# Optimization experiments

Measured on AMD Instinct MI355X. Metric: run time of the kernel, lower is better.

## Reference

```python
import jax, jax.numpy as jnp
import numpy as np
import math

HASHMAP_SIZE = 1 << 17
N_LEVELS = 16
N_FEATURES = 2
BASE_RES = 16.0
GROWTH = 1.5  # per-level resolution growth factor
PRIME_Y = np.uint32(2654435761)  # Instant-NGP spatial hash prime


def hash_encode(x, encoding):
    """Multiresolution 2D hash-grid encoding with bilinear interpolation.
    x: [N, 2] in [0,1); encoding: [T, L, F]. Returns [N, L*F]."""
    N = x.shape[0]
    scales = jnp.asarray(BASE_RES * GROWTH ** np.arange(N_LEVELS),
                         dtype=x.dtype)  # [L]
    pos = x[:, None, :] * scales[None, :, None]        # [N, L, 2]
    pf = jnp.floor(pos)
    frac = pos - pf                                    # [N, L, 2]
    pi = pf.astype(jnp.uint32)                         # integer corner base
    lvl = jnp.arange(N_LEVELS)[None, :]                # [1, L]

    feat = jnp.zeros((N, N_LEVELS, N_FEATURES), dtype=x.dtype)
    for cx in (0, 1):
        for cy in (0, 1):
            ix = pi[..., 0] + jnp.uint32(cx)
            iy = pi[..., 1] + jnp.uint32(cy)
            h = ix ^ (iy * PRIME_Y)                    # spatial hash (wraps mod 2^32)
            idx = (h & jnp.uint32(HASHMAP_SIZE - 1)).astype(jnp.int32)  # [N, L]
            wx = frac[..., 0] if cx else 1.0 - frac[..., 0]
            wy = frac[..., 1] if cy else 1.0 - frac[..., 1]
            feat = feat + (wx * wy)[..., None] * encoding[idx, lvl]  # gather [N,L,F]
    return feat.reshape(N, N_LEVELS * N_FEATURES)


def setup_inputs() -> dict:
    key = jax.random.key(0)
    ks = jax.random.split(key, 8)
    N = 1 << 20
    n_neurons = [32, 64, 64, 3]
    x = jax.random.uniform(ks[0], (N, 2), dtype=jnp.float32)
    # encoding init: rand * 2e-4 - 1e-4
    encoding = jax.random.uniform(ks[1], (HASHMAP_SIZE, N_LEVELS, N_FEATURES),
                                  dtype=jnp.float32) * 2e-4 - 1e-4
    inp = {"x": x, "encoding": encoding}
    for i in range(3):
        s = 1.0 / math.sqrt(n_neurons[i])
        w = jax.random.uniform(ks[2 + i], (n_neurons[i], n_neurons[i + 1]),
                               dtype=jnp.float32) * 2 * s - s
        b = jax.random.uniform(ks[5 + i], (n_neurons[i + 1],),
                               dtype=jnp.float32) * 2 * s - s
        inp[f"w{i}"] = w
        inp[f"b{i}"] = b
    return inp


def reference(x, encoding, w0, b0, w1, b1, w2, b2):
    feat = hash_encode(x, encoding)                 # [N, 32]
    h = jax.nn.relu(feat @ w0 + b0)                 # [N, 64]
    h = jax.nn.relu(h @ w1 + b1)                    # [N, 64]
    return h @ w2 + b2                              # [N, 3]
```

## Files before the change

### kernel.cpp

```cpp
#include <hip/hip_runtime.h>
#include <stdint.h>

typedef __bf16 bf16_t;
typedef bf16_t bf16x8 __attribute__((ext_vector_type(8)));
typedef float  f32x4  __attribute__((ext_vector_type(4)));
typedef float  f32x2v __attribute__((ext_vector_type(2)));

static constexpr uint32_t PRIME = 2654435761u;
static constexpr uint32_t HMASK = (1u << 17) - 1u;
static constexpr uint32_t TSIZE = 1u << 17;

static constexpr int NLDS   = 5308;
static constexpr int NDALL  = 136642;

static constexpr float FSCALE = 8192.0f;
static constexpr float WSCALE = 1.0f / 8192.0f;

__device__ __forceinline__ uint32_t fbits(float f) {
    union { float f; uint32_t u; } v; v.f = f; return v.u;
}
__device__ __forceinline__ float asfloat(uint32_t u) {
    union { uint32_t u; float f; } v; v.u = u; return v.f;
}

__device__ __forceinline__ uint32_t enc8(float v) {
    const uint32_t s = (fbits(v) >> 24) & 0x80u;
    float m = fabsf(v) * 0x1p-120f;
    uint32_t u = fbits(m);
    u += 0x7FFFFu + ((u >> 20) & 1u);
    return s | ((u >> 20) & 0x7fu);
}
__device__ __forceinline__ uint32_t pack8(float a, float b) {
#if __has_builtin(__builtin_amdgcn_cvt_pk_fp8_f32)
    return (uint32_t)__builtin_amdgcn_cvt_pk_fp8_f32(a, b, 0, false) & 0xffffu;
#else
    return enc8(a) | (enc8(b) << 8);
#endif
}
template <bool HI>
__device__ __forceinline__ float2 unpack8w(uint32_t u) {
#if __has_builtin(__builtin_amdgcn_cvt_pk_f32_fp8)
    f32x2v r = __builtin_amdgcn_cvt_pk_f32_fp8((int)u, HI);
    return make_float2(r.x, r.y);
#else
    const uint32_t w = HI ? (u >> 16) : (u & 0xffffu);
    const float f0 = asfloat(((w & 0x80u) << 24) | ((w & 0x7fu) << 20)) * 0x1p120f;
    const float f1 = asfloat(((w & 0x8000u) << 16) | ((w & 0x7f00u) << 12)) * 0x1p120f;
    return make_float2(f0, f1);
#endif
}

__global__ __launch_bounds__(256)
void prepass_all(const float2* __restrict__ src, uint16_t* __restrict__ tab8,
                 uint16_t* __restrict__ dense) {
    __shared__ uint16_t ldsT[8 * 257];
    const int tid = threadIdx.x;
    if (blockIdx.x < 512) {
        const int t0 = blockIdx.x * 256;
#pragma unroll
        for (int k = 0; k < 8; ++k) {
            const int j = k * 256 + tid;
            const int tl = j >> 3, l8 = j & 7;
            const float2 f = src[((size_t)(t0 + tl) << 4) + 8 + l8];
            ldsT[l8 * 257 + tl] = (uint16_t)pack8(f.x * FSCALE, f.y * FSCALE);
        }
        __syncthreads();
#pragma unroll
        for (int k = 0; k < 8; ++k)
            tab8[((uint32_t)k << 17) + t0 + tid] = ldsT[k * 257 + tid];
    } else {
        const int i = (blockIdx.x - 512) * 256 + tid;
        if (i >= NDALL) return;
        int lvl, W, off;
        if      (i <   289) { lvl = 0; W =  17; off = 0;     }
        else if (i <   914) { lvl = 1; W =  25; off = 289;   }
        else if (i <  2283) { lvl = 2; W =  37; off = 914;   }
        else if (i <  5308) { lvl = 3; W =  55; off = 2283;  }
        else if (i < 12032) { lvl = 4; W =  82; off = 5308;  }
        else if (i < 27161) { lvl = 5; W = 123; off = 12032; }
        else if (i < 61017) { lvl = 6; W = 184; off = 27161; }
        else                { lvl = 7; W = 275; off = 61017; }
        const int li = i - off;
        const uint32_t iy = (uint32_t)(li / W), ix = (uint32_t)(li % W);
        const uint32_t h = (ix ^ (iy * PRIME)) & HMASK;
        const float2 f = src[h * 16 + lvl];
        dense[i] = (uint16_t)pack8(f.x * FSCALE, f.y * FSCALE);
    }
}

__global__ __launch_bounds__(256, 2)
void fused_hash_mlp(const float* __restrict__ xin,
                    const uint16_t* __restrict__ tab8,
                    const uint16_t* __restrict__ dense,
                    const float* __restrict__ w0, const float* __restrict__ b0,
                    const float* __restrict__ w1, const float* __restrict__ b1,
                    const float* __restrict__ w2, const float* __restrict__ b2,
                    float* __restrict__ out,
                    int nGroups)
{
    __shared__ uint16_t ldsTab[NLDS];
    __shared__ __align__(16) bf16_t lds[4 * 16 * 64];

    const int tid  = threadIdx.x;
    const int wib  = tid >> 6;
    const int lane = tid & 63;
    const int q    = lane >> 4;
    const int n16  = lane & 15;
    const int m7   = n16 & 7;
    const int mb   = n16 >> 3;

    bf16_t* myLds = &lds[wib * (16 * 64)];

    for (int i = tid; i < NLDS; i += 256) ldsTab[i] = dense[i];

    bf16x8 Bw0[4], Bw1[2][4], Bw2[2];
#pragma unroll
    for (int t = 0; t < 4; ++t)
#pragma unroll
        for (int j = 0; j < 8; ++j)
            Bw0[t][j] = (bf16_t)(w0[(q * 8 + j) * 64 + t * 16 + n16] * WSCALE);
#pragma unroll
    for (int c = 0; c < 2; ++c)
#pragma unroll
        for (int t = 0; t < 4; ++t)
#pragma unroll
            for (int j = 0; j < 8; ++j)
                Bw1[c][t][j] = (bf16_t)w1[(c * 32 + q * 8 + j) * 64 + t * 16 + n16];
#pragma unroll
    for (int c = 0; c < 2; ++c)
#pragma unroll
        for (int j = 0; j < 8; ++j)
            Bw2[c][j] = (n16 < 3) ? (bf16_t)w2[(c * 32 + q * 8 + j) * 3 + n16]
                                  : (bf16_t)0.0f;

    float bv0[4], bv1[4];
#pragma unroll
    for (int t = 0; t < 4; ++t) {
        bv0[t] = b0[t * 16 + n16];
        bv1[t] = b1[t * 16 + n16];
    }
    const float bv2 = (n16 < 3) ? b2[n16] : 0.0f;

    const float sb = 16.0f * ((q == 0) ? 1.0f :
                              (q == 1) ? 5.0625f :
                              (q == 2) ? 25.62890625f :
                                         129.746337890625f);
    const float sc[4] = { sb, sb * 1.5f, sb * 2.25f, sb * 3.375f };

    const uint32_t l8base = ((uint32_t)((q >= 2 ? q - 2 : 0) * 4)) << 17;

    int wbase[4];
#pragma unroll
    for (int r = 0; r < 4; ++r)
        wbase[r] = (q * 4 + r) * 64 + m7 + ((mb ^ (r & 1)) << 3) + ((q & 1) << 5);
    const int rIdx0 = n16 * 64 + (( q      ^ m7) << 3);
    const int rIdx1 = n16 * 64 + (((4 + q) ^ m7) << 3);

    __syncthreads();

    for (int g = blockIdx.x; g < nGroups; g += gridDim.x) {
        const int tile = g * 4 + wib;
        const int p = tile * 16 + n16;
        const float2 xy = ((const float2*)xin)[p];
        const float px = xy.x, py = xy.y;

        bf16x8 af;
#pragma unroll
        for (int lv = 0; lv < 4; ++lv) {
            const float posx = px * sc[lv], posy = py * sc[lv];
            const float fx = floorf(posx), fy = floorf(posy);
            const float frx = posx - fx,  fry = posy - fy;
            const uint32_t ix = (uint32_t)fx, iy = (uint32_t)fy;

            const uint32_t Wl = (lv == 0) ? 17u  : (lv == 1) ? 25u
                              : (lv == 2) ? 37u  : 55u;
            const uint32_t Ol = (lv == 0) ? 0u   : (lv == 1) ? 289u
                              : (lv == 2) ? 914u : 2283u;
            const uint32_t Wg = (lv == 0) ? 82u    : (lv == 1) ? 123u
                              : (lv == 2) ? 184u   : 275u;
            const uint32_t Og = (lv == 0) ? 5308u  : (lv == 1) ? 12032u
                              : (lv == 2) ? 27161u : 61017u;

            uint32_t u00, u10, u01, u11;
            if (q == 0) {
                const uint32_t a = Ol + iy * Wl + ix;
                u00 = ldsTab[a];
                u10 = ldsTab[a + 1];
                u01 = ldsTab[a + Wl];
                u11 = ldsTab[a + Wl + 1];
            } else if (q == 1) {
                const uint32_t a = Og + iy * Wg + ix;
                u00 = dense[a];
                u10 = dense[a + 1];
                u01 = dense[a + Wg];
                u11 = dense[a + Wg + 1];
            } else {
                const uint32_t hy0 = iy * PRIME, hy1 = hy0 + PRIME;
                const uint32_t i00 = ( ix       ^ hy0) & HMASK;
                const uint32_t i10 = ((ix + 1u) ^ hy0) & HMASK;
                const uint32_t i01 = ( ix       ^ hy1) & HMASK;
                const uint32_t i11 = ((ix + 1u) ^ hy1) & HMASK;
                const uint32_t base = l8base + ((uint32_t)lv << 17);
                u00 = tab8[base + i00];
                u10 = tab8[base + i10];
                u01 = tab8[base + i01];
                u11 = tab8[base + i11];
            }

            const float2 e00 = unpack8w<false>(u00);
            const float2 e10 = unpack8w<false>(u10);
            const float2 e01 = unpack8w<false>(u01);
            const float2 e11 = unpack8w<false>(u11);
            const float wx1 = frx, wx0 = 1.0f - frx, wy1 = fry, wy0 = 1.0f - fry;
            const float w00 = wx0 * wy0, w10 = wx1 * wy0, w01 = wx0 * wy1, w11 = wx1 * wy1;
            const float f0 = w00 * e00.x + w10 * e10.x + w01 * e01.x + w11 * e11.x;
            const float f1 = w00 * e00.y + w10 * e10.y + w01 * e01.y + w11 * e11.y;
            af[2 * lv]     = (bf16_t)f0;
            af[2 * lv + 1] = (bf16_t)f1;
        }

        f32x4 c0[4];
#pragma unroll
        for (int t = 0; t < 4; ++t) {
            f32x4 cc = { bv0[t], bv0[t], bv0[t], bv0[t] };
            c0[t] = __builtin_amdgcn_mfma_f32_16x16x32_bf16(af, Bw0[t], cc, 0, 0, 0);
        }

#pragma unroll
        for (int t = 0; t < 4; ++t)
#pragma unroll
            for (int r = 0; r < 4; ++r) {
                const int idx = ((t < 2) ? wbase[r] : (wbase[r] ^ 32))
                              + ((((t & 1) ^ ((r >> 1) & 1))) << 4);
                myLds[idx] = (bf16_t)fmaxf(c0[t][r], 0.0f);
            }
        bf16x8 A1[2];
        A1[0] = *(const bf16x8*)&myLds[rIdx0];
        A1[1] = *(const bf16x8*)&myLds[rIdx1];

        f32x4 c1[4];
#pragma unroll
        for (int t = 0; t < 4; ++t) {
            f32x4 cc = { bv1[t], bv1[t], bv1[t], bv1[t] };
            cc    = __builtin_amdgcn_mfma_f32_16x16x32_bf16(A1[0], Bw1[0][t], cc, 0, 0, 0);
            c1[t] = __builtin_amdgcn_mfma_f32_16x16x32_bf16(A1[1], Bw1[1][t], cc, 0, 0, 0);
        }

#pragma unroll
        for (int t = 0; t < 4; ++t)
#pragma unroll
            for (int r = 0; r < 4; ++r) {
                const int idx = ((t < 2) ? wbase[r] : (wbase[r] ^ 32))
                              + ((((t & 1) ^ ((r >> 1) & 1))) << 4);
                myLds[idx] = (bf16_t)fmaxf(c1[t][r], 0.0f);
            }
        bf16x8 A2[2];
        A2[0] = *(const bf16x8*)&myLds[rIdx0];
        A2[1] = *(const bf16x8*)&myLds[rIdx1];

        f32x4 co = { bv2, bv2, bv2, bv2 };
        co = __builtin_amdgcn_mfma_f32_16x16x32_bf16(A2[0], Bw2[0], co, 0, 0, 0);
        co = __builtin_amdgcn_mfma_f32_16x16x32_bf16(A2[1], Bw2[1], co, 0, 0, 0);

        if (n16 < 3) {
#pragma unroll
            for (int r = 0; r < 4; ++r)
                out[(size_t)(tile * 16 + q * 4 + r) * 3 + n16] = co[r];
        }
    }
}

__global__ __launch_bounds__(256)
void fused_hash_mlp_fp32(const float* __restrict__ xin,
                         const float* __restrict__ enc,
                         const float* __restrict__ w0, const float* __restrict__ b0,
                         const float* __restrict__ w1, const float* __restrict__ b1,
                         const float* __restrict__ w2, const float* __restrict__ b2,
                         float* __restrict__ out,
                         int nGroups)
{
    __shared__ __align__(16) bf16_t lds[4 * 16 * 80];
    const int tid  = threadIdx.x;
    const int wib  = tid >> 6;
    const int lane = tid & 63;
    const int q    = lane >> 4;
    const int n16  = lane & 15;
    bf16_t* myLds = &lds[wib * (16 * 80)];

    bf16x8 Bw0[4], Bw1[2][4], Bw2[2];
#pragma unroll
    for (int t = 0; t < 4; ++t)
#pragma unroll
        for (int j = 0; j < 8; ++j)
            Bw0[t][j] = (bf16_t)w0[(q * 8 + j) * 64 + t * 16 + n16];
#pragma unroll
    for (int c = 0; c < 2; ++c)
#pragma unroll
        for (int t = 0; t < 4; ++t)
#pragma unroll
            for (int j = 0; j < 8; ++j)
                Bw1[c][t][j] = (bf16_t)w1[(c * 32 + q * 8 + j) * 64 + t * 16 + n16];
#pragma unroll
    for (int c = 0; c < 2; ++c)
#pragma unroll
        for (int j = 0; j < 8; ++j)
            Bw2[c][j] = (n16 < 3) ? (bf16_t)w2[(c * 32 + q * 8 + j) * 3 + n16]
                                  : (bf16_t)0.0f;

    float bv0[4], bv1[4];
#pragma unroll
    for (int t = 0; t < 4; ++t) { bv0[t] = b0[t * 16 + n16]; bv1[t] = b1[t * 16 + n16]; }
    const float bv2 = (n16 < 3) ? b2[n16] : 0.0f;

    const float sb = 16.0f * ((q == 0) ? 1.0f : (q == 1) ? 5.0625f :
                              (q == 2) ? 25.62890625f : 129.746337890625f);
    const float sc[4] = { sb, sb * 1.5f, sb * 2.25f, sb * 3.375f };
    const char* encB = (const char*)enc;
    const uint32_t lvBase = (uint32_t)q * 32u;

    for (int g = blockIdx.x; g < nGroups; g += gridDim.x) {
        const int tile = g * 4 + wib;
        const int p = tile * 16 + n16;
        const float2 xy = ((const float2*)xin)[p];
        const float px = xy.x, py = xy.y;

        bf16x8 af;
#pragma unroll
        for (int lv = 0; lv < 4; ++lv) {
            const float posx = px * sc[lv], posy = py * sc[lv];
            const float fx = floorf(posx), fy = floorf(posy);
            const float frx = posx - fx,  fry = posy - fy;
            const uint32_t ix = (uint32_t)fx, iy = (uint32_t)fy;
            const uint32_t hy0 = iy * PRIME, hy1 = hy0 + PRIME;
            const uint32_t i00 = ( ix       ^ hy0) & HMASK;
            const uint32_t i10 = ((ix + 1u) ^ hy0) & HMASK;
            const uint32_t i01 = ( ix       ^ hy1) & HMASK;
            const uint32_t i11 = ((ix + 1u) ^ hy1) & HMASK;
            const uint32_t off = lvBase + (uint32_t)lv * 8u;
            const float2 e00 = *(const float2*)(encB + (i00 * 128u + off));
            const float2 e10 = *(const float2*)(encB + (i10 * 128u + off));
            const float2 e01 = *(const float2*)(encB + (i01 * 128u + off));
            const float2 e11 = *(const float2*)(encB + (i11 * 128u + off));
            const float wx1 = frx, wx0 = 1.0f - frx, wy1 = fry, wy0 = 1.0f - fry;
            const float w00 = wx0 * wy0, w10 = wx1 * wy0, w01 = wx0 * wy1, w11 = wx1 * wy1;
            af[2 * lv]     = (bf16_t)(w00 * e00.x + w10 * e10.x + w01 * e01.x + w11 * e11.x);
            af[2 * lv + 1] = (bf16_t)(w00 * e00.y + w10 * e10.y + w01 * e01.y + w11 * e11.y);
        }

        f32x4 c0[4];
#pragma unroll
        for (int t = 0; t < 4; ++t) {
            f32x4 cc = { bv0[t], bv0[t], bv0[t], bv0[t] };
            c0[t] = __builtin_amdgcn_mfma_f32_16x16x32_bf16(af, Bw0[t], cc, 0, 0, 0);
        }
        __syncthreads();
#pragma unroll
        for (int t = 0; t < 4; ++t)
#pragma unroll
            for (int r = 0; r < 4; ++r)
                myLds[(q * 4 + r) * 80 + t * 16 + n16] = (bf16_t)fmaxf(c0[t][r], 0.0f);
        __syncthreads();
        bf16x8 A1[2];
#pragma unroll
        for (int c = 0; c < 2; ++c)
            A1[c] = *(const bf16x8*)&myLds[n16 * 80 + c * 32 + q * 8];

        f32x4 c1[4];
#pragma unroll
        for (int t = 0; t < 4; ++t) {
            f32x4 cc = { bv1[t], bv1[t], bv1[t], bv1[t] };
            cc    = __builtin_amdgcn_mfma_f32_16x16x32_bf16(A1[0], Bw1[0][t], cc, 0, 0, 0);
            c1[t] = __builtin_amdgcn_mfma_f32_16x16x32_bf16(A1[1], Bw1[1][t], cc, 0, 0, 0);
        }
        __syncthreads();
#pragma unroll
        for (int t = 0; t < 4; ++t)
#pragma unroll
            for (int r = 0; r < 4; ++r)
                myLds[(q * 4 + r) * 80 + t * 16 + n16] = (bf16_t)fmaxf(c1[t][r], 0.0f);
        __syncthreads();
        bf16x8 A2[2];
#pragma unroll
        for (int c = 0; c < 2; ++c)
            A2[c] = *(const bf16x8*)&myLds[n16 * 80 + c * 32 + q * 8];

        f32x4 co = { bv2, bv2, bv2, bv2 };
        co = __builtin_amdgcn_mfma_f32_16x16x32_bf16(A2[0], Bw2[0], co, 0, 0, 0);
        co = __builtin_amdgcn_mfma_f32_16x16x32_bf16(A2[1], Bw2[1], co, 0, 0, 0);
        if (n16 < 3) {
#pragma unroll
            for (int r = 0; r < 4; ++r)
                out[(size_t)(tile * 16 + q * 4 + r) * 3 + n16] = co[r];
        }
    }
}

extern "C" void kernel_launch(void* const* d_in, const int* in_sizes, int n_in,
                              void* d_out, int out_size, void* d_ws, size_t ws_size,
                              hipStream_t stream) {
    const float* x  = (const float*)d_in[0];
    const float* en = (const float*)d_in[1];
    const float* w0 = (const float*)d_in[2];
    const float* b0 = (const float*)d_in[3];
    const float* w1 = (const float*)d_in[4];
    const float* b1 = (const float*)d_in[5];
    const float* w2 = (const float*)d_in[6];
    const float* b2 = (const float*)d_in[7];
    float* out = (float*)d_out;

    const int N = in_sizes[0] / 2;
    const int nTiles = N / 16;
    const int nGroups = nTiles / 4;

    const size_t wsNeeded = ((size_t)TSIZE * 8 + NDALL) * 2;
    if (ws_size >= wsNeeded) {
        uint16_t* tab8  = (uint16_t*)d_ws;
        uint16_t* dense = tab8 + ((size_t)TSIZE * 8);
        const int preBlocks = 512 + (NDALL + 255) / 256;
        prepass_all<<<preBlocks, 256, 0, stream>>>((const float2*)en, tab8, dense);
        int blocks = 2048;
        if (blocks > nGroups) blocks = nGroups;
        fused_hash_mlp<<<blocks, 256, 0, stream>>>(x, tab8, dense,
                                                   w0, b0, w1, b1, w2, b2, out, nGroups);
    } else {
        int blocks = 2048;
        if (blocks > nGroups) blocks = nGroups;
        fused_hash_mlp_fp32<<<blocks, 256, 0, stream>>>(x, en, w0, b0, w1, b1, w2, b2, out, nGroups);
    }
}
```

Measured before the change: 198.9 us.

## Stage MLP weights in LDS and raise occupancy target to cut VGPR pressure

Result: slower. 493.5 us (+148.1%).

```diff
diff --git a/kernel.cpp b/kernel.cpp
--- a/kernel.cpp
+++ b/kernel.cpp
@@ -10,7 +10,6 @@
 static constexpr uint32_t HMASK = (1u << 17) - 1u;
 static constexpr uint32_t TSIZE = 1u << 17;
 
-static constexpr int NLDS   = 5308;
 static constexpr int NDALL  = 136642;
 
 static constexpr float FSCALE = 8192.0f;
@@ -88,7 +87,7 @@
     }
 }
 
-__global__ __launch_bounds__(256, 2)
+__global__ __launch_bounds__(256, 8)
 void fused_hash_mlp(const float* __restrict__ xin,
                     const uint16_t* __restrict__ tab8,
                     const uint16_t* __restrict__ dense,
@@ -98,8 +97,8 @@
                     float* __restrict__ out,
                     int nGroups)
 {
-    __shared__ uint16_t ldsTab[NLDS];
     __shared__ __align__(16) bf16_t lds[4 * 16 * 64];
+    __shared__ __align__(16) bf16_t wLds[12 * 64 * 8];
 
     const int tid  = threadIdx.x;
     const int wib  = tid >> 6;
@@ -111,28 +110,33 @@
 
     bf16_t* myLds = &lds[wib * (16 * 64)];
 
-    for (int i = tid; i < NLDS; i += 256) ldsTab[i] = dense[i];
-
-    bf16x8 Bw0[4], Bw1[2][4], Bw2[2];
-#pragma unroll
-    for (int t = 0; t < 4; ++t)
-#pragma unroll
-        for (int j = 0; j < 8; ++j)
-            Bw0[t][j] = (bf16_t)(w0[(q * 8 + j) * 64 + t * 16 + n16] * WSCALE);
-#pragma unroll
-    for (int c = 0; c < 2; ++c)
-#pragma unroll
-        for (int t = 0; t < 4; ++t)
+    {
+        bf16x8 tmp;
+#pragma unroll
+        for (int t = 0; t < 4; ++t) {
 #pragma unroll
             for (int j = 0; j < 8; ++j)
-                Bw1[c][t][j] = (bf16_t)w1[(c * 32 + q * 8 + j) * 64 + t * 16 + n16];
+                tmp[j] = (bf16_t)(w0[(q * 8 + j) * 64 + t * 16 + n16] * WSCALE);
+            if (wib == 0) *(bf16x8*)&wLds[(t * 64 + lane) * 8] = tmp;
+        }
+#pragma unroll
+        for (int c = 0; c < 2; ++c)
+#pragma unroll
+            for (int t = 0; t < 4; ++t) {
+#pragma unroll
+                for (int j = 0; j < 8; ++j)
+                    tmp[j] = (bf16_t)w1[(c * 32 + q * 8 + j) * 64 + t * 16 + n16];
+                if (wib == 0) *(bf16x8*)&wLds[((4 + c * 4 + t) * 64 + lane) * 8] = tmp;
+            }
+    }
+
+    bf16x8 Bw2[2];
 #pragma unroll
     for (int c = 0; c < 2; ++c)
 #pragma unroll
         for (int j = 0; j < 8; ++j)
             Bw2[c][j] = (n16 < 3) ? (bf16_t)w2[(c * 32 + q * 8 + j) * 3 + n16]
                                   : (bf16_t)0.0f;
-
     float bv0[4], bv1[4];
 #pragma unroll
     for (int t = 0; t < 4; ++t) {
@@ -182,18 +186,14 @@
                               : (lv == 2) ? 27161u : 61017u;
 
             uint32_t u00, u10, u01, u11;
-            if (q == 0) {
-                const uint32_t a = Ol + iy * Wl + ix;
-                u00 = ldsTab[a];
-                u10 = ldsTab[a + 1];
-                u01 = ldsTab[a + Wl];
-                u11 = ldsTab[a + Wl + 1];
-            } else if (q == 1) {
-                const uint32_t a = Og + iy * Wg + ix;
+            if (q < 2) {
+                const uint32_t W = (q == 0) ? Wl : Wg;
+                const uint32_t O = (q == 0) ? Ol : Og;
+                const uint32_t a = O + iy * W + ix;
                 u00 = dense[a];
                 u10 = dense[a + 1];
-                u01 = dense[a + Wg];
-                u11 = dense[a + Wg + 1];
+                u01 = dense[a + W];
+                u11 = dense[a + W + 1];
             } else {
                 const uint32_t hy0 = iy * PRIME, hy1 = hy0 + PRIME;
                 const uint32_t i00 = ( ix       ^ hy0) & HMASK;
@@ -219,41 +219,36 @@
             af[2 * lv + 1] = (bf16_t)f1;
         }
 
-        f32x4 c0[4];
 #pragma unroll
         for (int t = 0; t < 4; ++t) {
+            const bf16x8 bw = *(const bf16x8*)&wLds[(t * 64 + lane) * 8];
             f32x4 cc = { bv0[t], bv0[t], bv0[t], bv0[t] };
-            c0[t] = __builtin_amdgcn_mfma_f32_16x16x32_bf16(af, Bw0[t], cc, 0, 0, 0);
-        }
-
-#pragma unroll
-        for (int t = 0; t < 4; ++t)
+            cc = __builtin_amdgcn_mfma_f32_16x16x32_bf16(af, bw, cc, 0, 0, 0);
 #pragma unroll
             for (int r = 0; r < 4; ++r) {
                 const int idx = ((t < 2) ? wbase[r] : (wbase[r] ^ 32))
                               + ((((t & 1) ^ ((r >> 1) & 1))) << 4);
-                myLds[idx] = (bf16_t)fmaxf(c0[t][r], 0.0f);
+                myLds[idx] = (bf16_t)fmaxf(cc[r], 0.0f);
             }
+        }
         bf16x8 A1[2];
         A1[0] = *(const bf16x8*)&myLds[rIdx0];
         A1[1] = *(const bf16x8*)&myLds[rIdx1];
 
-        f32x4 c1[4];
 #pragma unroll
         for (int t = 0; t < 4; ++t) {
+            const bf16x8 bwa = *(const bf16x8*)&wLds[((4 + t) * 64 + lane) * 8];
+            const bf16x8 bwb = *(const bf16x8*)&wLds[((8 + t) * 64 + lane) * 8];
             f32x4 cc = { bv1[t], bv1[t], bv1[t], bv1[t] };
-            cc    = __builtin_amdgcn_mfma_f32_16x16x32_bf16(A1[0], Bw1[0][t], cc, 0, 0, 0);
-            c1[t] = __builtin_amdgcn_mfma_f32_16x16x32_bf16(A1[1], Bw1[1][t], cc, 0, 0, 0);
-        }
-
-#pragma unroll
-        for (int t = 0; t < 4; ++t)
+            cc = __builtin_amdgcn_mfma_f32_16x16x32_bf16(A1[0], bwa, cc, 0, 0, 0);
+            cc = __builtin_amdgcn_mfma_f32_16x16x32_bf16(A1[1], bwb, cc, 0, 0, 0);
 #pragma unroll
             for (int r = 0; r < 4; ++r) {
                 const int idx = ((t < 2) ? wbase[r] : (wbase[r] ^ 32))
                               + ((((t & 1) ^ ((r >> 1) & 1))) << 4);
-                myLds[idx] = (bf16_t)fmaxf(c1[t][r], 0.0f);
+                myLds[idx] = (bf16_t)fmaxf(cc[r], 0.0f);
             }
+        }
         bf16x8 A2[2];
         A2[0] = *(const bf16x8*)&myLds[rIdx0];
         A2[1] = *(const bf16x8*)&myLds[rIdx1];
```

## Split fused hash-MLP into separate encode and MLP kernels via workspace features

Applied to the files above, without the earlier changes.

Measured after the change: 232.3 us. 16.8% more time.

```diff
diff --git a/kernel.cpp b/kernel.cpp
--- a/kernel.cpp
+++ b/kernel.cpp
@@ -88,6 +88,210 @@
     }
 }
 
+
+__global__ __launch_bounds__(256, 4)
+void encode_feat(const float* __restrict__ xin,
+                 const uint16_t* __restrict__ tab8,
+                 const uint16_t* __restrict__ dense,
+                 bf16_t* __restrict__ feat,
+                 int nGroups)
+{
+    const int tid  = threadIdx.x;
+    const int wib  = tid >> 6;
+    const int lane = tid & 63;
+    const int q    = lane >> 4;
+    const int n16  = lane & 15;
+
+    const float sb = 16.0f * ((q == 0) ? 1.0f :
+                              (q == 1) ? 5.0625f :
+                              (q == 2) ? 25.62890625f :
+                                         129.746337890625f);
+    const float sc[4] = { sb, sb * 1.5f, sb * 2.25f, sb * 3.375f };
+    const uint32_t l8base = ((uint32_t)((q >= 2 ? q - 2 : 0) * 4)) << 17;
+
+    for (int g = blockIdx.x; g < nGroups; g += gridDim.x) {
+        const int p = (g * 4 + wib) * 16 + n16;
+        const float2 xy = ((const float2*)xin)[p];
+        const float px = xy.x, py = xy.y;
+
+        bf16x8 af;
+#pragma unroll
+        for (int lv = 0; lv < 4; ++lv) {
+            const float posx = px * sc[lv], posy = py * sc[lv];
+            const float fx = floorf(posx), fy = floorf(posy);
+            const float frx = posx - fx,  fry = posy - fy;
+            const uint32_t ix = (uint32_t)fx, iy = (uint32_t)fy;
+
+            const uint32_t Wl = (lv == 0) ? 17u  : (lv == 1) ? 25u
+                              : (lv == 2) ? 37u  : 55u;
+            const uint32_t Ol = (lv == 0) ? 0u   : (lv == 1) ? 289u
+                              : (lv == 2) ? 914u : 2283u;
+            const uint32_t Wg = (lv == 0) ? 82u    : (lv == 1) ? 123u
+                              : (lv == 2) ? 184u   : 275u;
+            const uint32_t Og = (lv == 0) ? 5308u  : (lv == 1) ? 12032u
+                              : (lv == 2) ? 27161u : 61017u;
+
+            uint32_t u00, u10, u01, u11;
+            if (q < 2) {
+                const uint32_t W = (q == 0) ? Wl : Wg;
+                const uint32_t O = (q == 0) ? Ol : Og;
+                const uint32_t a = O + iy * W + ix;
+                u00 = dense[a];
+                u10 = dense[a + 1];
+                u01 = dense[a + W];
+                u11 = dense[a + W + 1];
+            } else {
+                const uint32_t hy0 = iy * PRIME, hy1 = hy0 + PRIME;
+                const uint32_t i00 = ( ix       ^ hy0) & HMASK;
+                const uint32_t i10 = ((ix + 1u) ^ hy0) & HMASK;
+                const uint32_t i01 = ( ix       ^ hy1) & HMASK;
+                const uint32_t i11 = ((ix + 1u) ^ hy1) & HMASK;
+                const uint32_t base = l8base + ((uint32_t)lv << 17);
+                u00 = tab8[base + i00];
+                u10 = tab8[base + i10];
+                u01 = tab8[base + i01];
+                u11 = tab8[base + i11];
+            }
+
+            const float2 e00 = unpack8w<false>(u00);
+            const float2 e10 = unpack8w<false>(u10);
+            const float2 e01 = unpack8w<false>(u01);
+            const float2 e11 = unpack8w<false>(u11);
+            const float wx1 = frx, wx0 = 1.0f - frx, wy1 = fry, wy0 = 1.0f - fry;
+            const float w00 = wx0 * wy0, w10 = wx1 * wy0, w01 = wx0 * wy1, w11 = wx1 * wy1;
+            const float f0 = w00 * e00.x + w10 * e10.x + w01 * e01.x + w11 * e11.x;
+            const float f1 = w00 * e00.y + w10 * e10.y + w01 * e01.y + w11 * e11.y;
+            af[2 * lv]     = (bf16_t)f0;
+            af[2 * lv + 1] = (bf16_t)f1;
+        }
+
+        *(bf16x8*)&feat[(size_t)p * 32 + q * 8] = af;
+    }
+}
+
+__global__ __launch_bounds__(256, 2)
+void mlp_feat(const bf16_t* __restrict__ feat,
+              const float* __restrict__ w0, const float* __restrict__ b0,
+              const float* __restrict__ w1, const float* __restrict__ b1,
+              const float* __restrict__ w2, const float* __restrict__ b2,
+              float* __restrict__ out,
+              int nGroups)
+{
+    __shared__ __align__(16) bf16_t lds[4 * 16 * 64];
+
+    const int tid  = threadIdx.x;
+    const int wib  = tid >> 6;
+    const int lane = tid & 63;
+    const int q    = lane >> 4;
+    const int n16  = lane & 15;
+    const int m7   = n16 & 7;
+    const int mb   = n16 >> 3;
+
+    bf16_t* myLds = &lds[wib * (16 * 64)];
+
+    bf16x8 Bw0[4], Bw1[2][4], Bw2[2];
+#pragma unroll
+    for (int t = 0; t < 4; ++t)
+#pragma unroll
+        for (int j = 0; j < 8; ++j)
+            Bw0[t][j] = (bf16_t)(w0[(q * 8 + j) * 64 + t * 16 + n16] * WSCALE);
+#pragma unroll
+    for (int c = 0; c < 2; ++c)
+#pragma unroll
+        for (int t = 0; t < 4; ++t)
+#pragma unroll
+            for (int j = 0; j < 8; ++j)
+                Bw1[c][t][j] = (bf16_t)w1[(c * 32 + q * 8 + j) * 64 + t * 16 + n16];
+#pragma unroll
+    for (int c = 0; c < 2; ++c)
+#pragma unroll
+        for (int j = 0; j < 8; ++j)
+            Bw2[c][j] = (n16 < 3) ? (bf16_t)w2[(c * 32 + q * 8 + j) * 3 + n16]
+                                  : (bf16_t)0.0f;
+
+    float bv0[4], bv1[4];
+#pragma unroll
+    for (int t = 0; t < 4; ++t) {
+        bv0[t] = b0[t * 16 + n16];
+        bv1[t] = b1[t * 16 + n16];
+    }
+    const float bv2 = (n16 < 3) ? b2[n16] : 0.0f;
+
+    int wbase[4];
+#pragma unroll
+    for (int r = 0; r < 4; ++r)
+        wbase[r] = (q * 4 + r) * 64 + m7 + ((mb ^ (r & 1)) << 3) + ((q & 1) << 5);
+    const int rIdx0 = n16 * 64 + (( q      ^ m7) << 3);
+    const int rIdx1 = n16 * 64 + (((4 + q) ^ m7) << 3);
+
+    const int gLast = nGroups - 1;
+    int g = blockIdx.x;
+    if (g > gLast) return;
+
+    auto ldaf = [&](int gg) -> bf16x8 {
+        const size_t p = (size_t)(gg * 4 + wib) * 16 + n16;
+        return *(const bf16x8*)&feat[p * 32 + q * 8];
+    };
+
+    bf16x8 af = ldaf(g);
+
+    for (; g <= gLast; g += gridDim.x) {
+        int gN = g + gridDim.x; if (gN > gLast) gN = gLast;
+        const bf16x8 afN = ldaf(gN);
+
+        const int tile = g * 4 + wib;
+
+        f32x4 c0[4];
+#pragma unroll
+        for (int t = 0; t < 4; ++t) {
+            f32x4 cc = { bv0[t], bv0[t], bv0[t], bv0[t] };
+            c0[t] = __builtin_amdgcn_mfma_f32_16x16x32_bf16(af, Bw0[t], cc, 0, 0, 0);
+        }
+#pragma unroll
+        for (int t = 0; t < 4; ++t)
+#pragma unroll
+            for (int r = 0; r < 4; ++r) {
+                const int idx = ((t < 2) ? wbase[r] : (wbase[r] ^ 32))
+                              + ((((t & 1) ^ ((r >> 1) & 1))) << 4);
+                myLds[idx] = (bf16_t)fmaxf(c0[t][r], 0.0f);
+            }
+        bf16x8 A1[2];
+        A1[0] = *(const bf16x8*)&myLds[rIdx0];
+        A1[1] = *(const bf16x8*)&myLds[rIdx1];
+
+        f32x4 c1[4];
+#pragma unroll
+        for (int t = 0; t < 4; ++t) {
+            f32x4 cc = { bv1[t], bv1[t], bv1[t], bv1[t] };
+            cc    = __builtin_amdgcn_mfma_f32_16x16x32_bf16(A1[0], Bw1[0][t], cc, 0, 0, 0);
+            c1[t] = __builtin_amdgcn_mfma_f32_16x16x32_bf16(A1[1], Bw1[1][t], cc, 0, 0, 0);
+        }
+#pragma unroll
+        for (int t = 0; t < 4; ++t)
+#pragma unroll
+            for (int r = 0; r < 4; ++r) {
+                const int idx = ((t < 2) ? wbase[r] : (wbase[r] ^ 32))
+                              + ((((t & 1) ^ ((r >> 1) & 1))) << 4);
+                myLds[idx] = (bf16_t)fmaxf(c1[t][r], 0.0f);
+            }
+        bf16x8 A2[2];
+        A2[0] = *(const bf16x8*)&myLds[rIdx0];
+        A2[1] = *(const bf16x8*)&myLds[rIdx1];
+
+        f32x4 co = { bv2, bv2, bv2, bv2 };
+        co = __builtin_amdgcn_mfma_f32_16x16x32_bf16(A2[0], Bw2[0], co, 0, 0, 0);
+        co = __builtin_amdgcn_mfma_f32_16x16x32_bf16(A2[1], Bw2[1], co, 0, 0, 0);
+
+        if (n16 < 3) {
+#pragma unroll
+            for (int r = 0; r < 4; ++r)
+                out[(size_t)(tile * 16 + q * 4 + r) * 3 + n16] = co[r];
+        }
+
+        af = afN;
+    }
+}
+
 __global__ __launch_bounds__(256, 2)
 void fused_hash_mlp(const float* __restrict__ xin,
                     const uint16_t* __restrict__ tab8,
@@ -146,7 +350,6 @@
                               (q == 2) ? 25.62890625f :
                                          129.746337890625f);
     const float sc[4] = { sb, sb * 1.5f, sb * 2.25f, sb * 3.375f };
-
     const uint32_t l8base = ((uint32_t)((q >= 2 ? q - 2 : 0) * 4)) << 17;
 
     int wbase[4];
@@ -225,7 +428,6 @@
             f32x4 cc = { bv0[t], bv0[t], bv0[t], bv0[t] };
             c0[t] = __builtin_amdgcn_mfma_f32_16x16x32_bf16(af, Bw0[t], cc, 0, 0, 0);
         }
-
 #pragma unroll
         for (int t = 0; t < 4; ++t)
 #pragma unroll
@@ -245,7 +447,6 @@
             cc    = __builtin_amdgcn_mfma_f32_16x16x32_bf16(A1[0], Bw1[0][t], cc, 0, 0, 0);
             c1[t] = __builtin_amdgcn_mfma_f32_16x16x32_bf16(A1[1], Bw1[1][t], cc, 0, 0, 0);
         }
-
 #pragma unroll
         for (int t = 0; t < 4; ++t)
 #pragma unroll
@@ -412,11 +613,27 @@
     const int nTiles = N / 16;
     const int nGroups = nTiles / 4;
 
-    const size_t wsNeeded = ((size_t)TSIZE * 8 + NDALL) * 2;
-    if (ws_size >= wsNeeded) {
+    const size_t tabBytes   = (size_t)TSIZE * 8 * 2;
+    const size_t denseBytes = (size_t)NDALL * 2;
+    const size_t featOff    = (tabBytes + denseBytes + 255) & ~(size_t)255;
+    const size_t featBytes  = (size_t)N * 32 * 2;
+    const size_t wsSplit    = featOff + featBytes;
+    const size_t wsFused    = tabBytes + denseBytes;
+
+    const int preBlocks = 512 + (NDALL + 255) / 256;
+
+    if (ws_size >= wsSplit) {
         uint16_t* tab8  = (uint16_t*)d_ws;
-        uint16_t* dense = tab8 + ((size_t)TSIZE * 8);
-        const int preBlocks = 512 + (NDALL + 255) / 256;
+        uint16_t* dense = (uint16_t*)((char*)d_ws + tabBytes);
+        bf16_t*   feat  = (bf16_t*)((char*)d_ws + featOff);
+        prepass_all<<<preBlocks, 256, 0, stream>>>((const float2*)en, tab8, dense);
+        int blocks = 2048;
+        if (blocks > nGroups) blocks = nGroups;
+        encode_feat<<<blocks, 256, 0, stream>>>(x, tab8, dense, feat, nGroups);
+        mlp_feat<<<blocks, 256, 0, stream>>>(feat, w0, b0, w1, b1, w2, b2, out, nGroups);
+    } else if (ws_size >= wsFused) {
+        uint16_t* tab8  = (uint16_t*)d_ws;
+        uint16_t* dense = (uint16_t*)((char*)d_ws + tabBytes);
         prepass_all<<<preBlocks, 256, 0, stream>>>((const float2*)en, tab8, dense);
         int blocks = 2048;
         if (blocks > nGroups) blocks = nGroups;
```
